# Optimization experiments

Measured on AMD Instinct MI355X. Metric: run time of the kernel, lower is better.

Reference implementation:

```python
import jax, jax.numpy as jnp
import numpy as np

B, N, C, H = 2, 2048, 1024, 16
D = C // H  # head_dim = 64


def setup_inputs() -> dict:
    key = jax.random.key(0)
    ks = jax.random.split(key, 5)
    s = 0.02
    return {
        "x": jax.random.normal(ks[0], (B, N, C), dtype=jnp.float32),
        "w_qkv": jax.random.normal(ks[1], (3 * C, C), dtype=jnp.float32) * s,
        "b_qkv": jnp.zeros((3 * C,), dtype=jnp.float32),
        "w_proj": jax.random.normal(ks[2], (C, C), dtype=jnp.float32) * s,
        "b_proj": jnp.zeros((C,), dtype=jnp.float32),
    }


def reference(x, w_qkv, b_qkv, w_proj, b_proj):
    scale = D ** -0.5
    # QKV projection: [B,N,3C]
    qkv = jnp.einsum('bnc,oc->bno', x, w_qkv) + b_qkv
    qkv = qkv.reshape(B, N, 3, H, D).transpose(2, 0, 3, 1, 4)  # [3,B,H,N,D]
    q, k, v = qkv[0], qkv[1], qkv[2]
    attn = jnp.einsum('bhnd,bhmd->bhnm', q, k) * scale  # [B,H,N,N]
    attn = jax.nn.softmax(attn, axis=-1)
    out = jnp.einsum('bhnm,bhmd->bhnd', attn, v)  # [B,H,N,D]
    out = out.transpose(0, 2, 1, 3).reshape(B, N, C)
    return jnp.einsum('bnc,oc->bno', out, w_proj) + b_proj
```

## Files before the change

kernel.cpp:

```cpp
#include <hip/hip_runtime.h>
#include <hip/hip_bf16.h>

typedef __attribute__((ext_vector_type(4))) float f32x4;
typedef __attribute__((ext_vector_type(16))) float f32x16;
typedef __attribute__((ext_vector_type(8))) short short8;
typedef __attribute__((ext_vector_type(4))) unsigned int u32x4;
typedef __attribute__((ext_vector_type(2))) unsigned int u32x2;
typedef unsigned short u16;

__device__ __forceinline__ u16 f2bf(float x) {
  unsigned u = __float_as_uint(x);
  u += 0x7fffu + ((u >> 16) & 1u);
  return (u16)(u >> 16);
}

__device__ __forceinline__ void gload_lds16(const void* g, void* l) {
  __builtin_amdgcn_global_load_lds(
      (__attribute__((address_space(1))) void*)g,
      (__attribute__((address_space(3))) void*)l, 16, 0, 0);
}

__global__ void cvt_all(const float* __restrict__ x, const float* __restrict__ wq,
                        const float* __restrict__ wp, ushort4* __restrict__ dst) {
  const int N1 = 1048576, N2 = 786432, NT = 2097152;
  for (int i = blockIdx.x * 256 + threadIdx.x; i < NT; i += 524288) {
    float4 v;
    if (i < N1)            v = ((const float4*)x)[i];
    else if (i < N1 + N2)  v = ((const float4*)wq)[i - N1];
    else                   v = ((const float4*)wp)[i - N1 - N2];
    ushort4 o;
    o.x = f2bf(v.x); o.y = f2bf(v.y); o.z = f2bf(v.z); o.w = f2bf(v.w);
    dst[i] = o;
  }
}

__global__ __launch_bounds__(512, 2) void gemm256_bt(
    const u16* __restrict__ A, const u16* __restrict__ B,
    const float* __restrict__ bias, u16* __restrict__ Cout,
    int M, int N, int K, int nbx)
{
  __shared__ u16 LA[2][2][8192];
  __shared__ u16 LB[2][2][8192];

  const int tid  = threadIdx.x;
  const int w    = tid >> 6;
  const int lane = tid & 63;
  const int wm   = w >> 2;
  const int wn   = w & 3;
  const int hi   = lane >> 4;
  const int lo   = lane & 15;

  const int L  = (int)(blockIdx.x & 7) * ((int)gridDim.x >> 3) + (int)(blockIdx.x >> 3);
  const int bx = L / 16, by = L % 16;
  const long brow = (long)by * 256;
  const long bcol = (long)bx * 256;

  f32x4 acc[8][4];
#pragma unroll
  for (int m = 0; m < 8; ++m)
#pragma unroll
    for (int n = 0; n < 4; ++n)
#pragma unroll
      for (int r = 0; r < 4; ++r) acc[m][n][r] = 0.0f;

  const int srow = lane >> 3;
  const int sg   = (lane & 7) ^ srow;
  const int l7   = lo & 7;

  auto stA = [&](int kt, int bi, int i) {
    const long k0 = (long)kt * 64;
#pragma unroll
    for (int mh = 0; mh < 2; ++mh) {
      const long r = brow + mh * 128 + i * 64 + w * 8 + srow;
      gload_lds16(A + r * K + k0 + sg * 8, &LA[bi][mh][i * 4096 + w * 512]);
    }
  };
  auto stB = [&](int kt, int bi, int i) {
    const long k0 = (long)kt * 64;
#pragma unroll
    for (int nh = 0; nh < 2; ++nh) {
      const long r = bcol + nh * 128 + i * 64 + w * 8 + srow;
      gload_lds16(B + r * K + k0 + sg * 8, &LB[bi][nh][i * 4096 + w * 512]);
    }
  };

  short8 a[4][2], b0[2][2], b1[2][2];
  auto rdA = [&](int bi, int mq) {
#pragma unroll
    for (int f = 0; f < 4; ++f) {
      const int rl = mq * 64 + f * 16 + lo;
#pragma unroll
      for (int ks = 0; ks < 2; ++ks)
        a[f][ks] = *(const short8*)(&LA[bi][wm][rl * 64 + ((ks * 4 + hi) ^ l7) * 8]);
    }
  };
  auto rdB = [&](int bi, int nq, short8 bb[2][2]) {
#pragma unroll
    for (int f = 0; f < 2; ++f) {
      const int rl = (wn & 1) * 64 + nq * 32 + f * 16 + lo;
#pragma unroll
      for (int ks = 0; ks < 2; ++ks)
        bb[f][ks] = *(const short8*)(&LB[bi][wn >> 1][rl * 64 + ((ks * 4 + hi) ^ l7) * 8]);
    }
  };

#define MFMA16(mq, nq, BB)                                                          \
  __builtin_amdgcn_s_setprio(1);                                                    \
  _Pragma("unroll")                                                                 \
  for (int f = 0; f < 4; ++f)                                                       \
    _Pragma("unroll")                                                               \
    for (int n = 0; n < 2; ++n)                                                     \
      _Pragma("unroll")                                                             \
      for (int ks = 0; ks < 2; ++ks)                                                \
        acc[(mq)*4 + f][(nq)*2 + n] = __builtin_amdgcn_mfma_f32_16x16x32_bf16(      \
            a[f][ks], BB[n][ks], acc[(mq)*4 + f][(nq)*2 + n], 0, 0, 0);             \
  __builtin_amdgcn_s_setprio(0);

#define PHASE_WAIT()                                      \
  __builtin_amdgcn_s_barrier();                           \
  asm volatile("s_waitcnt lgkmcnt(0)" ::: "memory");      \
  __builtin_amdgcn_sched_barrier(0);

  const int nkt = K >> 6;
  stA(0, 0, 0); stA(0, 0, 1); stB(0, 0, 0); stB(0, 0, 1);
  stA(1, 1, 0); stA(1, 1, 1); stB(1, 1, 0); stB(1, 1, 1);
  asm volatile("s_waitcnt vmcnt(8)" ::: "memory");
  __builtin_amdgcn_s_barrier();

  for (int it = 0; it < (nkt >> 1); ++it) {
    const int t0 = it * 2;
    const bool pf = (t0 + 2 < nkt);
    rdA(0, 0); rdB(0, 0, b0);
    PHASE_WAIT(); MFMA16(0, 0, b0); __builtin_amdgcn_s_barrier();
    rdB(0, 1, b1);
    if (pf) stA(t0 + 2, 0, 0);
    PHASE_WAIT(); MFMA16(0, 1, b1); __builtin_amdgcn_s_barrier();
    rdA(0, 1);
    if (pf) stB(t0 + 2, 0, 0);
    PHASE_WAIT(); MFMA16(1, 0, b0); __builtin_amdgcn_s_barrier();
    if (pf) { stA(t0 + 2, 0, 1); stB(t0 + 2, 0, 1); }
    MFMA16(1, 1, b1);
    if (pf) { asm volatile("s_waitcnt vmcnt(8)" ::: "memory"); }
    else    { asm volatile("s_waitcnt vmcnt(0)" ::: "memory"); }
    __builtin_amdgcn_sched_barrier(0);
    __builtin_amdgcn_s_barrier();
    rdA(1, 0); rdB(1, 0, b0);
    PHASE_WAIT(); MFMA16(0, 0, b0); __builtin_amdgcn_s_barrier();
    rdB(1, 1, b1);
    if (pf) stA(t0 + 3, 1, 0);
    PHASE_WAIT(); MFMA16(0, 1, b1); __builtin_amdgcn_s_barrier();
    rdA(1, 1);
    if (pf) stB(t0 + 3, 1, 0);
    PHASE_WAIT(); MFMA16(1, 0, b0); __builtin_amdgcn_s_barrier();
    if (pf) { stA(t0 + 3, 1, 1); stB(t0 + 3, 1, 1); }
    MFMA16(1, 1, b1);
    if (pf) { asm volatile("s_waitcnt vmcnt(8)" ::: "memory"); }
    __builtin_amdgcn_sched_barrier(0);
    __builtin_amdgcn_s_barrier();
  }
#undef MFMA16
#undef PHASE_WAIT

  const float qsc = (bcol < 1024) ? 0.18033688011112042f : 1.0f;
  float bv[4];
#pragma unroll
  for (int n = 0; n < 4; ++n) bv[n] = bias[bcol + wn * 64 + n * 16 + lo];
#pragma unroll
  for (int m = 0; m < 8; ++m)
#pragma unroll
    for (int n = 0; n < 4; ++n)
#pragma unroll
      for (int r = 0; r < 4; ++r) {
        const long row = brow + wm * 128 + m * 16 + hi * 4 + r;
        const long col = bcol + wn * 64 + n * 16 + lo;
        Cout[row * (long)N + col] = f2bf((acc[m][n][r] + bv[n]) * qsc);
      }
}

template<int OUT_BF16>
__global__ __launch_bounds__(256) void gemm_bt(
    const u16* __restrict__ A, const u16* __restrict__ B,
    const float* __restrict__ bias, void* __restrict__ Cout,
    int M, int N, int K)
{
  __shared__ u16 As[2][128 * 64];
  __shared__ u16 Bs[2][128 * 64];
  const int tid  = threadIdx.x;
  const int lane = tid & 63;
  const int w    = tid >> 6;
  const int wm   = w >> 1, wn = w & 1;
  const int hi   = lane >> 4;
  const int lo   = lane & 15;
  const int l7   = lo & 7;
  const long brow = (long)blockIdx.y * 128;
  const long bcol = (long)blockIdx.x * 128;

  f32x4 acc[4][4];
#pragma unroll
  for (int i = 0; i < 4; i++)
#pragma unroll
    for (int j = 0; j < 4; j++)
#pragma unroll
      for (int r = 0; r < 4; r++) acc[i][j][r] = 0.0f;

  const int srow = lane >> 3;
  const int sg   = (lane & 7) ^ srow;

  float bv[4];
#pragma unroll
  for (int fn = 0; fn < 4; fn++) bv[fn] = bias[bcol + wn * 64 + fn * 16 + lo];

  auto stage = [&](int kt, int bi) {
    const int k0 = kt << 6;
#pragma unroll
    for (int c = 0; c < 4; ++c) {
      const int chunk = (c << 2) + w;
      const int ra = (chunk << 3) + srow;
      gload_lds16(A + (size_t)(brow + ra) * K + k0 + sg * 8, &As[bi][chunk * 512]);
      gload_lds16(B + (size_t)(bcol + ra) * K + k0 + sg * 8, &Bs[bi][chunk * 512]);
    }
  };

  const int nkt = K >> 6;
  stage(0, 0);
  __syncthreads();
  int cur = 0;

  for (int kt = 0; kt < nkt; ++kt) {
    if (kt + 1 < nkt) stage(kt + 1, cur ^ 1);
#pragma unroll
    for (int ks = 0; ks < 2; ++ks) {
      short8 af[4], bfr[4];
      const int g = ((ks * 4 + hi) ^ l7) * 8;
#pragma unroll
      for (int f = 0; f < 4; f++) {
        af[f]  = *(const short8*)(&As[cur][(wm * 64 + f * 16 + lo) * 64 + g]);
        bfr[f] = *(const short8*)(&Bs[cur][(wn * 64 + f * 16 + lo) * 64 + g]);
      }
#pragma unroll
      for (int fm = 0; fm < 4; fm++)
#pragma unroll
        for (int fn = 0; fn < 4; fn++)
          acc[fm][fn] = __builtin_amdgcn_mfma_f32_16x16x32_bf16(af[fm], bfr[fn], acc[fm][fn], 0, 0, 0);
    }
    __syncthreads();
    cur ^= 1;
  }

#pragma unroll
  for (int fm = 0; fm < 4; fm++)
#pragma unroll
    for (int fn = 0; fn < 4; fn++)
#pragma unroll
      for (int r = 0; r < 4; r++) {
        const long row = brow + wm * 64 + fm * 16 + hi * 4 + r;
        const long col = bcol + wn * 64 + fn * 16 + lo;
        const float v = acc[fm][fn][r] + bv[fn];
        if (OUT_BF16) ((u16*)Cout)[row * (long)N + col] = f2bf(v);
        else          ((float*)Cout)[row * (long)N + col] = v;
      }
}

__global__ __launch_bounds__(512, 4) void attn_fused(
    const u16* __restrict__ qkv, u16* __restrict__ out)
{
  __shared__ __align__(16) char smem[65536];

  const int tid  = threadIdx.x;
  const int w    = tid >> 6;
  const int lane = tid & 63;
  const int l31  = lane & 31;
  const int hc   = lane >> 5;
  const int g1   = (lane >> 4) & 1;
  const int l15  = lane & 15;
  const int half = w >> 2;
  const int qg   = w & 3;

  const int bid  = blockIdx.x;
  const int xcd  = bid & 7;
  const int slot = bid >> 3;
  const int qb   = slot & 15;
  const int bh   = ((slot >> 4) << 3) | xcd;
  const int b    = bh >> 4, h = bh & 15;

  short8 qf[4];
  {
    const u16* qp = qkv + (size_t)(b * 2048 + qb * 128 + qg * 32 + l31) * 3072 + h * 64 + hc * 8;
#pragma unroll
    for (int ds = 0; ds < 4; ++ds) qf[ds] = *(const short8*)(qp + ds * 16);
  }

  f32x16 acc0, acc1;
#pragma unroll
  for (int r = 0; r < 16; ++r) { acc0[r] = 0.f; acc1[r] = 0.f; }
  float lsum = 0.f;

  const int srow8 = lane >> 3;
  const int kgl   = (lane & 7) ^ srow8;
  const int vkey  = (lane >> 5) * 4 + ((lane >> 1) & 3);
  const int vd    = ((lane >> 3) & 3) * 16 + (lane & 1) * 8;

  auto kbuf = [&](int bi) { return (u16*)(smem + (size_t)(half * 2 + bi) * 8192); };
  auto vbuf = [&](int bi) { return (u16*)(smem + 32768 + (size_t)(half * 2 + bi) * 8192); };

  auto stage = [&](int t, int bi) {
    const size_t rbase = (size_t)(b * 2048 + half * 1024 + t * 64);
    u16* Kb = kbuf(bi);
    u16* Vb = vbuf(bi);
#pragma unroll
    for (int c = 0; c < 2; ++c) {
      const int chunk = qg * 2 + c;
      gload_lds16(qkv + (rbase + chunk * 8 + srow8) * 3072 + 1024 + h * 64 + kgl * 8,
                  Kb + chunk * 512);
      gload_lds16(qkv + (rbase + chunk * 8 + vkey) * 3072 + 2048 + h * 64 + vd,
                  Vb + chunk * 512);
    }
  };

  stage(0, 0);
  __syncthreads();
  int cur = 0;

  for (int t = 0; t < 16; ++t) {
    if (t < 15) stage(t + 1, cur ^ 1);

    const u16* Kc = kbuf(cur);
    const unsigned va =
        (unsigned)(unsigned long long)(const __attribute__((address_space(3))) u16*)vbuf(cur);

    f32x16 s0, s1;
#pragma unroll
    for (int r = 0; r < 16; ++r) { s0[r] = 0.f; s1[r] = 0.f; }
    __builtin_amdgcn_s_setprio(1);
#pragma unroll
    for (int ds = 0; ds < 4; ++ds) {
      const int gb = (((2 * ds + hc) ^ (lane & 7)) << 4);
      const short8 k0 = *(const short8*)((const char*)Kc + l31 * 128 + gb);
      const short8 k1 = *(const short8*)((const char*)Kc + 4096 + l31 * 128 + gb);
      s0 = __builtin_amdgcn_mfma_f32_32x32x16_bf16(k0, qf[ds], s0, 0, 0, 0);
      s1 = __builtin_amdgcn_mfma_f32_32x32x16_bf16(k1, qf[ds], s1, 0, 0, 0);
    }
    __builtin_amdgcn_s_setprio(0);

    float p[32];
#pragma unroll
    for (int r = 0; r < 16; ++r) {
      p[r]      = __builtin_amdgcn_exp2f(s0[r]);
      p[16 + r] = __builtin_amdgcn_exp2f(s1[r]);
    }
    {
      float a0 = 0.f, a1 = 0.f, a2 = 0.f, a3 = 0.f;
#pragma unroll
      for (int r = 0; r < 8; ++r) {
        a0 += p[r]; a1 += p[8 + r]; a2 += p[16 + r]; a3 += p[24 + r];
      }
      lsum += (a0 + a1) + (a2 + a3);
    }

    short8 pa[4];
#pragma unroll
    for (int ks = 0; ks < 4; ++ks) {
      const int bs = ks * 8;
      unsigned X0, X1, X2, X3;
      asm("v_cvt_pk_bf16_f32 %0, %1, %2" : "=v"(X0) : "v"(p[bs + 0]), "v"(p[bs + 1]));
      asm("v_cvt_pk_bf16_f32 %0, %1, %2" : "=v"(X1) : "v"(p[bs + 2]), "v"(p[bs + 3]));
      asm("v_cvt_pk_bf16_f32 %0, %1, %2" : "=v"(X2) : "v"(p[bs + 4]), "v"(p[bs + 5]));
      asm("v_cvt_pk_bf16_f32 %0, %1, %2" : "=v"(X3) : "v"(p[bs + 6]), "v"(p[bs + 7]));
      asm("v_permlane32_swap_b32 %0, %1" : "+v"(X0), "+v"(X2));
      asm("v_permlane32_swap_b32 %0, %1" : "+v"(X1), "+v"(X3));
      u32x4 wv;
      wv[0] = X0; wv[1] = X1; wv[2] = X2; wv[3] = X3;
      pa[ks] = __builtin_bit_cast(short8, wv);
    }

#pragma unroll
    for (int dt = 0; dt < 2; ++dt) {
      const unsigned vb = va + (unsigned)(hc * 1024 + dt * 256 + g1 * 128 + l15 * 8);
      u32x2 q0, q1, q2, q3, q4, q5, q6, q7;
      asm volatile("ds_read_b64_tr_b16 %0, %1"             : "=v"(q0) : "v"(vb));
      asm volatile("ds_read_b64_tr_b16 %0, %1 offset:512"  : "=v"(q1) : "v"(vb));
      asm volatile("ds_read_b64_tr_b16 %0, %1 offset:2048" : "=v"(q2) : "v"(vb));
      asm volatile("ds_read_b64_tr_b16 %0, %1 offset:2560" : "=v"(q3) : "v"(vb));
      asm volatile("ds_read_b64_tr_b16 %0, %1 offset:4096" : "=v"(q4) : "v"(vb));
      asm volatile("ds_read_b64_tr_b16 %0, %1 offset:4608" : "=v"(q5) : "v"(vb));
      asm volatile("ds_read_b64_tr_b16 %0, %1 offset:6144" : "=v"(q6) : "v"(vb));
      asm volatile("ds_read_b64_tr_b16 %0, %1 offset:6656" : "=v"(q7) : "v"(vb));
      asm volatile("s_waitcnt lgkmcnt(0)" ::: "memory");
      __builtin_amdgcn_sched_barrier(0);
      __builtin_amdgcn_s_setprio(1);
      f32x16 A = dt ? acc1 : acc0;
      {
        u32x4 bb; bb[0] = q0[0]; bb[1] = q0[1]; bb[2] = q1[0]; bb[3] = q1[1];
        A = __builtin_amdgcn_mfma_f32_32x32x16_bf16(pa[0], __builtin_bit_cast(short8, bb), A, 0, 0, 0);
      }
      {
        u32x4 bb; bb[0] = q2[0]; bb[1] = q2[1]; bb[2] = q3[0]; bb[3] = q3[1];
        A = __builtin_amdgcn_mfma_f32_32x32x16_bf16(pa[1], __builtin_bit_cast(short8, bb), A, 0, 0, 0);
      }
      {
        u32x4 bb; bb[0] = q4[0]; bb[1] = q4[1]; bb[2] = q5[0]; bb[3] = q5[1];
        A = __builtin_amdgcn_mfma_f32_32x32x16_bf16(pa[2], __builtin_bit_cast(short8, bb), A, 0, 0, 0);
      }
      {
        u32x4 bb; bb[0] = q6[0]; bb[1] = q6[1]; bb[2] = q7[0]; bb[3] = q7[1];
        A = __builtin_amdgcn_mfma_f32_32x32x16_bf16(pa[3], __builtin_bit_cast(short8, bb), A, 0, 0, 0);
      }
      __builtin_amdgcn_s_setprio(0);
      if (dt) acc1 = A; else acc0 = A;
    }

    __syncthreads();
    cur ^= 1;
  }

  float ltot = lsum + __shfl_xor(lsum, 32);
  float* MG = (float*)smem;
  const int midx = (qg * 64 + lane) * 33;
  if (half == 1) {
#pragma unroll
    for (int r = 0; r < 16; ++r) { MG[midx + r] = acc0[r]; MG[midx + 16 + r] = acc1[r]; }
    MG[midx + 32] = ltot;
  }
  __syncthreads();
  if (half == 0) {
#pragma unroll
    for (int r = 0; r < 16; ++r) { acc0[r] += MG[midx + r]; acc1[r] += MG[midx + 16 + r]; }
    ltot += MG[midx + 32];
    const float inv = 1.0f / ltot;
    const size_t orow0 = (size_t)(b * 2048 + qb * 128 + qg * 32);
#pragma unroll
    for (int r = 0; r < 16; ++r) {
      const int rowq = (r & 3) + 8 * (r >> 2) + 4 * hc;
      const float ir = __shfl(inv, rowq);
      out[(orow0 + rowq) * 1024 + h * 64 + l31]      = f2bf(acc0[r] * ir);
      out[(orow0 + rowq) * 1024 + h * 64 + 32 + l31] = f2bf(acc1[r] * ir);
    }
  }
}

extern "C" void kernel_launch(void* const* d_in, const int* in_sizes, int n_in,
                              void* d_out, int out_size, void* d_ws, size_t ws_size,
                              hipStream_t stream) {
  const float* x      = (const float*)d_in[0];
  const float* w_qkv  = (const float*)d_in[1];
  const float* b_qkv  = (const float*)d_in[2];
  const float* w_proj = (const float*)d_in[3];
  const float* b_proj = (const float*)d_in[4];
  float* out = (float*)d_out;

  char* ws = (char*)d_ws;
  u16* xb     = (u16*)(ws);
  u16* wqkvb  = (u16*)(ws + (8ull  << 20));
  u16* wprojb = (u16*)(ws + (14ull << 20));
  u16* qkvb   = (u16*)(ws + (16ull << 20));
  u16* aob    = (u16*)(ws + (40ull << 20));

  cvt_all<<<2048, 256, 0, stream>>>(x, w_qkv, w_proj, (ushort4*)ws);

  gemm256_bt<<<192, 512, 0, stream>>>(xb, wqkvb, b_qkv, qkvb, 4096, 3072, 1024, 12);

  attn_fused<<<512, 512, 0, stream>>>(qkvb, aob);

  gemm_bt<0><<<dim3(8, 32), 256, 0, stream>>>(aob, wprojb, b_proj, out, 4096, 1024, 1024);
}
```

Measured before the change: 111.6 us.

## Retile QKV GEMM to 256x192 blocks for 256-block grid and restructured pipeline

Changes the QKV projection GEMM tile from 256x256 to 256x192, so the grid grows from 192 to 256 blocks and matches the CU count better. The B tile in LDS shrinks, each wave now covers 48 columns with 3 n-fragments, and the four-phase MFMA schedule becomes two phases per k-tile with reordered prefetch and waitcnt values. The q-scale choice moves to per-fragment granularity because 192-wide tiles can straddle the Q/K boundary at column 1024. The trade-off is lower arithmetic intensity per block and a more complex async-load wait accounting.

```diff
diff --git a/kernel.cpp b/kernel.cpp
--- a/kernel.cpp
+++ b/kernel.cpp
@@ -37,10 +37,10 @@
 __global__ __launch_bounds__(512, 2) void gemm256_bt(
     const u16* __restrict__ A, const u16* __restrict__ B,
     const float* __restrict__ bias, u16* __restrict__ Cout,
-    int M, int N, int K, int nbx)
+    int M, int N, int K)
 {
   __shared__ u16 LA[2][2][8192];
-  __shared__ u16 LB[2][2][8192];
+  __shared__ u16 LB[2][12288];
 
   const int tid  = threadIdx.x;
   const int w    = tid >> 6;
@@ -50,16 +50,16 @@
   const int hi   = lane >> 4;
   const int lo   = lane & 15;
 
-  const int L  = (int)(blockIdx.x & 7) * ((int)gridDim.x >> 3) + (int)(blockIdx.x >> 3);
-  const int bx = L / 16, by = L % 16;
+  const int L  = (int)(blockIdx.x & 7) * 32 + (int)(blockIdx.x >> 3);
+  const int bx = L >> 4, by = L & 15;
   const long brow = (long)by * 256;
-  const long bcol = (long)bx * 256;
-
-  f32x4 acc[8][4];
+  const long bcol = (long)bx * 192;
+
+  f32x4 acc[8][3];
 #pragma unroll
   for (int m = 0; m < 8; ++m)
 #pragma unroll
-    for (int n = 0; n < 4; ++n)
+    for (int n = 0; n < 3; ++n)
 #pragma unroll
       for (int r = 0; r < 4; ++r) acc[m][n][r] = 0.0f;
 
@@ -75,16 +75,13 @@
       gload_lds16(A + r * K + k0 + sg * 8, &LA[bi][mh][i * 4096 + w * 512]);
     }
   };
-  auto stB = [&](int kt, int bi, int i) {
+  auto stB = [&](int kt, int bi, int u) {
     const long k0 = (long)kt * 64;
-#pragma unroll
-    for (int nh = 0; nh < 2; ++nh) {
-      const long r = bcol + nh * 128 + i * 64 + w * 8 + srow;
-      gload_lds16(B + r * K + k0 + sg * 8, &LB[bi][nh][i * 4096 + w * 512]);
-    }
-  };
-
-  short8 a[4][2], b0[2][2], b1[2][2];
+    const long r = bcol + u * 64 + w * 8 + srow;
+    gload_lds16(B + r * K + k0 + sg * 8, &LB[bi][u * 4096 + w * 512]);
+  };
+
+  short8 a[4][2], b[3][2];
   auto rdA = [&](int bi, int mq) {
 #pragma unroll
     for (int f = 0; f < 4; ++f) {
@@ -94,26 +91,26 @@
         a[f][ks] = *(const short8*)(&LA[bi][wm][rl * 64 + ((ks * 4 + hi) ^ l7) * 8]);
     }
   };
-  auto rdB = [&](int bi, int nq, short8 bb[2][2]) {
-#pragma unroll
-    for (int f = 0; f < 2; ++f) {
-      const int rl = (wn & 1) * 64 + nq * 32 + f * 16 + lo;
+  auto rdB = [&](int bi) {
+#pragma unroll
+    for (int f = 0; f < 3; ++f) {
+      const int rl = wn * 48 + f * 16 + lo;
 #pragma unroll
       for (int ks = 0; ks < 2; ++ks)
-        bb[f][ks] = *(const short8*)(&LB[bi][wn >> 1][rl * 64 + ((ks * 4 + hi) ^ l7) * 8]);
-    }
-  };
-
-#define MFMA16(mq, nq, BB)                                                          \
+        b[f][ks] = *(const short8*)(&LB[bi][rl * 64 + ((ks * 4 + hi) ^ l7) * 8]);
+    }
+  };
+
+#define MFMA24(mq)                                                                  \
   __builtin_amdgcn_s_setprio(1);                                                    \
   _Pragma("unroll")                                                                 \
   for (int f = 0; f < 4; ++f)                                                       \
     _Pragma("unroll")                                                               \
-    for (int n = 0; n < 2; ++n)                                                     \
+    for (int n = 0; n < 3; ++n)                                                     \
       _Pragma("unroll")                                                             \
       for (int ks = 0; ks < 2; ++ks)                                                \
-        acc[(mq)*4 + f][(nq)*2 + n] = __builtin_amdgcn_mfma_f32_16x16x32_bf16(      \
-            a[f][ks], BB[n][ks], acc[(mq)*4 + f][(nq)*2 + n], 0, 0, 0);             \
+        acc[(mq)*4 + f][n] = __builtin_amdgcn_mfma_f32_16x16x32_bf16(               \
+            a[f][ks], b[n][ks], acc[(mq)*4 + f][n], 0, 0, 0);                       \
   __builtin_amdgcn_s_setprio(0);
 
 #define PHASE_WAIT()                                      \
@@ -122,59 +119,52 @@
   __builtin_amdgcn_sched_barrier(0);
 
   const int nkt = K >> 6;
-  stA(0, 0, 0); stA(0, 0, 1); stB(0, 0, 0); stB(0, 0, 1);
-  stA(1, 1, 0); stA(1, 1, 1); stB(1, 1, 0); stB(1, 1, 1);
-  asm volatile("s_waitcnt vmcnt(8)" ::: "memory");
+  stA(0, 0, 0); stA(0, 0, 1); stB(0, 0, 0); stB(0, 0, 1); stB(0, 0, 2);
+  stA(1, 1, 0); stA(1, 1, 1); stB(1, 1, 0); stB(1, 1, 1); stB(1, 1, 2);
+  asm volatile("s_waitcnt vmcnt(7)" ::: "memory");
   __builtin_amdgcn_s_barrier();
 
   for (int it = 0; it < (nkt >> 1); ++it) {
-    const int t0 = it * 2;
-    const bool pf = (t0 + 2 < nkt);
-    rdA(0, 0); rdB(0, 0, b0);
-    PHASE_WAIT(); MFMA16(0, 0, b0); __builtin_amdgcn_s_barrier();
-    rdB(0, 1, b1);
-    if (pf) stA(t0 + 2, 0, 0);
-    PHASE_WAIT(); MFMA16(0, 1, b1); __builtin_amdgcn_s_barrier();
+    const int t2 = 2 * it + 2, t3 = 2 * it + 3;
+    rdA(0, 0); rdB(0);
+    if (it > 0) stA(2 * it + 1, 1, 1);
+    PHASE_WAIT(); MFMA24(0); __builtin_amdgcn_s_barrier();
     rdA(0, 1);
-    if (pf) stB(t0 + 2, 0, 0);
-    PHASE_WAIT(); MFMA16(1, 0, b0); __builtin_amdgcn_s_barrier();
-    if (pf) { stA(t0 + 2, 0, 1); stB(t0 + 2, 0, 1); }
-    MFMA16(1, 1, b1);
-    if (pf) { asm volatile("s_waitcnt vmcnt(8)" ::: "memory"); }
-    else    { asm volatile("s_waitcnt vmcnt(0)" ::: "memory"); }
+    if (t2 < nkt) { stB(t2, 0, 0); stB(t2, 0, 1); stB(t2, 0, 2); stA(t2, 0, 0); }
+    PHASE_WAIT(); MFMA24(1);
+    if (t2 < nkt) { asm volatile("s_waitcnt vmcnt(5)" ::: "memory"); }
+    else          { asm volatile("s_waitcnt vmcnt(0)" ::: "memory"); }
     __builtin_amdgcn_sched_barrier(0);
     __builtin_amdgcn_s_barrier();
-    rdA(1, 0); rdB(1, 0, b0);
-    PHASE_WAIT(); MFMA16(0, 0, b0); __builtin_amdgcn_s_barrier();
-    rdB(1, 1, b1);
-    if (pf) stA(t0 + 3, 1, 0);
-    PHASE_WAIT(); MFMA16(0, 1, b1); __builtin_amdgcn_s_barrier();
+    rdA(1, 0); rdB(1);
+    if (t2 < nkt) stA(t2, 0, 1);
+    PHASE_WAIT(); MFMA24(0); __builtin_amdgcn_s_barrier();
     rdA(1, 1);
-    if (pf) stB(t0 + 3, 1, 0);
-    PHASE_WAIT(); MFMA16(1, 0, b0); __builtin_amdgcn_s_barrier();
-    if (pf) { stA(t0 + 3, 1, 1); stB(t0 + 3, 1, 1); }
-    MFMA16(1, 1, b1);
-    if (pf) { asm volatile("s_waitcnt vmcnt(8)" ::: "memory"); }
+    if (t3 < nkt) { stB(t3, 1, 0); stB(t3, 1, 1); stB(t3, 1, 2); stA(t3, 1, 0); }
+    PHASE_WAIT(); MFMA24(1);
+    if (t3 < nkt) { asm volatile("s_waitcnt vmcnt(5)" ::: "memory"); }
     __builtin_amdgcn_sched_barrier(0);
     __builtin_amdgcn_s_barrier();
   }
-#undef MFMA16
+#undef MFMA24
 #undef PHASE_WAIT
 
-  const float qsc = (bcol < 1024) ? 0.18033688011112042f : 1.0f;
-  float bv[4];
-#pragma unroll
-  for (int n = 0; n < 4; ++n) bv[n] = bias[bcol + wn * 64 + n * 16 + lo];
+  const float SCC = 0.18033688011112042f;
+  float bv[3];
+#pragma unroll
+  for (int n = 0; n < 3; ++n) bv[n] = bias[bcol + wn * 48 + n * 16 + lo];
 #pragma unroll
   for (int m = 0; m < 8; ++m)
 #pragma unroll
-    for (int n = 0; n < 4; ++n)
+    for (int n = 0; n < 3; ++n) {
+      const long colf = bcol + wn * 48 + n * 16;
+      const float qsc = (colf < 1024) ? SCC : 1.0f;
 #pragma unroll
       for (int r = 0; r < 4; ++r) {
         const long row = brow + wm * 128 + m * 16 + hi * 4 + r;
-        const long col = bcol + wn * 64 + n * 16 + lo;
-        Cout[row * (long)N + col] = f2bf((acc[m][n][r] + bv[n]) * qsc);
-      }
+        Cout[row * (long)N + colf + lo] = f2bf((acc[m][n][r] + bv[n]) * qsc);
+      }
+    }
 }
 
 template<int OUT_BF16>
@@ -457,7 +447,7 @@
 
   cvt_all<<<2048, 256, 0, stream>>>(x, w_qkv, w_proj, (ushort4*)ws);
 
-  gemm256_bt<<<192, 512, 0, stream>>>(xb, wqkvb, b_qkv, qkvb, 4096, 3072, 1024, 12);
+  gemm256_bt<<<256, 512, 0, stream>>>(xb, wqkvb, b_qkv, qkvb, 4096, 3072, 1024);
 
   attn_fused<<<512, 512, 0, stream>>>(qkvb, aob);
 
```

New measurement: 107.0 us. -4.1%, faster.
